# Kernel optimization log

Measured on AMD Instinct MI355X. Metric: run time of the kernel, lower is better.

## Reference

```python
import jax, jax.numpy as jnp
import numpy as np

B, S, I, H = 1024, 200, 4, 128  # batch, seq_len, interest_num, hidden_size
ROUTING_TIMES = 3
EPS = 1e-9


def setup_inputs() -> dict:
    key = jax.random.key(0)
    k1, k2, k3 = jax.random.split(key, 3)
    item_eb = jax.random.normal(k1, (B, S, H), dtype=jnp.float32)
    mask = jax.random.randint(k2, (B, S), 0, 2, dtype=jnp.int32)
    w = jax.random.normal(k3, (1, S, I * H, H), dtype=jnp.float32)
    return {"item_eb": item_eb, "mask": mask, "w": w}


def _squash_factor(cap):
    # cap: [B, I, 1, H]; standard capsule squash scale
    n = jnp.sum(jnp.square(cap), axis=-1, keepdims=True)
    return n / (1.0 + n) / jnp.sqrt(n + EPS)


def reference(item_eb, mask, w):
    # bilinear_type == 2: item_eb_hat[b,s,i] = sum_h w[0,s,i,h] * item_eb[b,s,h]
    hat = jnp.einsum('bsh,sjh->bsj', item_eb, w[0])          # [B, S, I*H]
    hat = hat.reshape(B, S, I, H).transpose(0, 2, 1, 3)      # [B, I, S, H]
    hat_iter = jax.lax.stop_gradient(hat)                    # stop_grad=True

    atten_mask = mask[:, None, :]                            # [B, 1, S] broadcasts over I
    capsule_weight = jnp.zeros((B, I, S), dtype=item_eb.dtype)

    interest_capsule = None
    for i in range(ROUTING_TIMES):
        sw = jax.nn.softmax(capsule_weight, axis=-1)         # [B, I, S]
        sw = jnp.where(atten_mask == 0, jnp.zeros_like(sw), sw)
        sw = sw[:, :, None, :]                               # [B, I, 1, S]
        src = hat_iter if i < ROUTING_TIMES - 1 else hat
        interest_capsule = jnp.matmul(sw, src)               # [B, I, 1, H]
        interest_capsule = _squash_factor(interest_capsule) * interest_capsule
        if i < ROUTING_TIMES - 1:
            # delta[b,i,s] = <hat_iter[b,i,s,:], capsule[b,i,0,:]>
            delta = jnp.matmul(hat_iter, jnp.swapaxes(interest_capsule, 2, 3))
            capsule_weight = capsule_weight + delta.reshape(B, I, S)

    return interest_capsule.reshape(B, I, H)
```

## Files before the change

### kernel.cpp

```cpp
#include <hip/hip_runtime.h>
#include <hip/hip_bf16.h>
#include <cstdint>

#define SDIM 200
#define HDIM 128
#define IDIM 4
#define BDIM 1024
#define LDK 72
#define REG_US 9216
#define HALF_US 18432
#define IMG_US 36864

typedef __attribute__((ext_vector_type(8))) short short8;
typedef __attribute__((ext_vector_type(4))) float f32x4;

__device__ __forceinline__ ushort f32_to_bf16u(float f) {
    uint32_t u = __builtin_bit_cast(uint32_t, f);
    u += 0x7FFFu + ((u >> 16) & 1u);
    return (ushort)(u >> 16);
}
__device__ __forceinline__ float bf16u_to_f32(ushort h) {
    uint32_t u = ((uint32_t)h) << 16;
    return __builtin_bit_cast(float, u);
}
__device__ __forceinline__ void split8(const float* p, uint4* hi, uint4* lo) {
    union { ushort u[8]; uint4 v; } xh, xl;
    #pragma unroll
    for (int j = 0; j < 8; ++j) {
        float f = p[j];
        ushort h = f32_to_bf16u(f);
        float r = f - bf16u_to_f32(h);
        xh.u[j] = h;
        xl.u[j] = f32_to_bf16u(r);
    }
    *hi = xh.v; *lo = xl.v;
}

__global__ __launch_bounds__(256) void wstage(const float* __restrict__ w,
                                              ushort* __restrict__ img) {
    const int blk = blockIdx.x;
    const int s = blk >> 2, ii = blk & 3;
    const int t = threadIdx.x;
    const float* wB = w + ((size_t)s * (IDIM * HDIM) + (size_t)ii * HDIM) * HDIM;
    ushort* dst = img + (size_t)blk * IMG_US;

    for (int g = t; g < 2048; g += 256) {
        uint4 hi, lo;
        split8(wB + (size_t)g * 8, &hi, &lo);
        int c0 = g >> 4;
        int st = (g >> 3) & 1;
        int kl = (g & 7) * 8;
        *(uint4*)(dst + st * HALF_US +          c0 * LDK + kl) = hi;
        *(uint4*)(dst + st * HALF_US + REG_US + c0 * LDK + kl) = lo;
    }
    for (int p = t; p < 4096; p += 256) {
        int rg = p >> 10, c0 = (p >> 3) & 127, o = p & 7;
        dst[rg * REG_US + c0 * LDK + 64 + o] = 0;
    }
}

__global__ __launch_bounds__(256) void hat_gemm(const float* __restrict__ item,
                                                const ushort* __restrict__ img,
                                                float* __restrict__ hat,
                                                int b0) {
    __shared__ ushort lds[HALF_US];

    const int blk = blockIdx.x;
    const int bt = blk / SDIM;
    const int s  = blk % SDIM;
    const int t  = threadIdx.x;
    const int wave = t >> 6, lane = t & 63;
    const int wm = wave >> 1, wn = wave & 1;
    const int m0 = lane & 15, q = lane >> 4;

    short8 ah[2][2][4], al[2][2][4];
    const float* ib = item +
        ((size_t)(b0 + bt * 128 + wm * 64 + m0) * SDIM + s) * HDIM;
    #pragma unroll
    for (int tm = 0; tm < 4; ++tm) {
        const float* p = ib + (size_t)(tm * 16) * (SDIM * HDIM);
        #pragma unroll
        for (int st = 0; st < 2; ++st)
            #pragma unroll
            for (int kk = 0; kk < 2; ++kk) {
                uint4 hi, lo;
                split8(p + st * 64 + kk * 32 + q * 8, &hi, &lo);
                ah[st][kk][tm] = __builtin_bit_cast(short8, hi);
                al[st][kk][tm] = __builtin_bit_cast(short8, lo);
            }
    }

    const ushort* imgS = img + (size_t)(s * IDIM) * IMG_US;

    #pragma unroll 1
    for (int ii = 0; ii < IDIM; ++ii) {
        const ushort* wimg = imgS + (size_t)ii * IMG_US;

        f32x4 acc[4][4];
        #pragma unroll
        for (int tm = 0; tm < 4; ++tm)
            #pragma unroll
            for (int tn = 0; tn < 4; ++tn)
                acc[tm][tn] = (f32x4){0.f, 0.f, 0.f, 0.f};

        #pragma unroll
        for (int st = 0; st < 2; ++st) {
            __syncthreads();

            {
                const uint4* src = (const uint4*)(wimg + (size_t)st * HALF_US);
                uint4* dstl = (uint4*)lds;
                #pragma unroll
                for (int k = 0; k < 9; ++k)
                    dstl[t + 256 * k] = src[t + 256 * k];
            }
            __syncthreads();

            const ushort* Wh = lds;
            const ushort* Wl = lds + REG_US;
            #pragma unroll
            for (int kk = 0; kk < 2; ++kk) {
                const int kof = kk * 32 + q * 8;
                short8 bh[4], bl[4];
                #pragma unroll
                for (int tn = 0; tn < 4; ++tn) {
                    int ro = (wn * 64 + tn * 16 + m0) * LDK + kof;
                    bh[tn] = *(const short8*)(&Wh[ro]);
                    bl[tn] = *(const short8*)(&Wl[ro]);
                }
                #pragma unroll
                for (int tm = 0; tm < 4; ++tm)
                    #pragma unroll
                    for (int tn = 0; tn < 4; ++tn) {
                        acc[tm][tn] = __builtin_amdgcn_mfma_f32_16x16x32_bf16(
                            ah[st][kk][tm], bl[tn], acc[tm][tn], 0, 0, 0);
                        acc[tm][tn] = __builtin_amdgcn_mfma_f32_16x16x32_bf16(
                            al[st][kk][tm], bh[tn], acc[tm][tn], 0, 0, 0);
                        acc[tm][tn] = __builtin_amdgcn_mfma_f32_16x16x32_bf16(
                            ah[st][kk][tm], bh[tn], acc[tm][tn], 0, 0, 0);
                    }
            }
        }

        #pragma unroll
        for (int tm = 0; tm < 4; ++tm) {
            #pragma unroll
            for (int tn = 0; tn < 4; ++tn) {
                const int col = wn * 64 + tn * 16 + m0;
                #pragma unroll
                for (int rg = 0; rg < 4; ++rg) {
                    const size_t bl_ = (size_t)(bt * 128 + wm * 64 + tm * 16 + q * 4 + rg);
                    hat[((bl_ * IDIM + ii) * SDIM + s) * HDIM + col] = acc[tm][tn][rg];
                }
            }
        }
    }
}

__global__ __launch_bounds__(512) void routing4(const float* __restrict__ hat,
                                                const int* __restrict__ mask,
                                                float* __restrict__ out, int b0) {
    __shared__ float cw[SDIM];
    __shared__ float icp[16 * HDIM];
    __shared__ float icf[HDIM];
    __shared__ int   mk[SDIM];

    const int blk = blockIdx.x;
    const int bl = blk >> 2, ii = blk & 3;
    const int b = b0 + bl;
    const int t = threadIdx.x, lane = t & 63, wv = t >> 6;
    const int hq = (t & 31) * 4;
    const int sg = t >> 5;
    const bool has13 = (sg < 8);
    const float* base = hat + ((size_t)bl * IDIM + ii) * (SDIM * HDIM);

    if (t < SDIM) mk[t] = mask[(size_t)b * SDIM + t];

    float4 pf[13];
    #pragma unroll
    for (int j = 0; j < 12; ++j)
        pf[j] = *(const float4*)(base + (size_t)(sg + 16 * j) * HDIM + hq);
    pf[12] = has13 ? *(const float4*)(base + (size_t)(sg + 192) * HDIM + hq)
                   : (float4){0.f, 0.f, 0.f, 0.f};
    __syncthreads();

    {
        float4 u = {0.f, 0.f, 0.f, 0.f};
        #pragma unroll
        for (int j = 0; j < 12; ++j) {
            if (mk[sg + 16 * j]) {
                u.x += pf[j].x; u.y += pf[j].y; u.z += pf[j].z; u.w += pf[j].w;
            }
        }
        if (has13 && mk[sg + 192]) {
            u.x += pf[12].x; u.y += pf[12].y; u.z += pf[12].z; u.w += pf[12].w;
        }
        *(float4*)(&icp[sg * HDIM + hq]) = u;
    }
    __syncthreads();
    {
        float i0 = 0.f, i1 = 0.f;
        #pragma unroll
        for (int g = 0; g < 16; ++g) {
            i0 += icp[g * HDIM + lane];
            i1 += icp[g * HDIM + lane + 64];
        }
        i0 *= (1.0f / 200.0f);
        i1 *= (1.0f / 200.0f);
        float p = i0 * i0 + i1 * i1;
        #pragma unroll
        for (int off = 32; off > 0; off >>= 1) p += __shfl_xor(p, off);
        float fac = p / (1.0f + p) / sqrtf(p + 1e-9f);
        if (wv == 0) {
            icf[lane] = i0 * fac;
            icf[lane + 64] = i1 * fac;
        }
    }
    __syncthreads();

    for (int iter = 1; iter <= 2; ++iter) {
        float4 c4 = *(const float4*)(&icf[hq]);
        #pragma unroll
        for (int j = 0; j < 13; ++j) {
            float d = fmaf(pf[j].x, c4.x, fmaf(pf[j].y, c4.y,
                      fmaf(pf[j].z, c4.z, pf[j].w * c4.w)));
            d += __shfl_xor(d, 16);
            d += __shfl_xor(d, 8);
            d += __shfl_xor(d, 4);
            d += __shfl_xor(d, 2);
            d += __shfl_xor(d, 1);
            if ((t & 31) == 0 && (j < 12 || has13)) {
                int s = sg + 16 * j;
                cw[s] = (iter == 1) ? d : cw[s] + d;
            }
        }
        __syncthreads();

        float m = fmaxf(cw[lane], fmaxf(cw[lane + 64], cw[lane + 128]));
        if (lane < SDIM - 192) m = fmaxf(m, cw[lane + 192]);
        #pragma unroll
        for (int off = 32; off > 0; off >>= 1) m = fmaxf(m, __shfl_xor(m, off));

        float D = __expf(cw[lane] - m) + __expf(cw[lane + 64] - m)
                + __expf(cw[lane + 128] - m)
                + ((lane < SDIM - 192) ? __expf(cw[lane + 192] - m) : 0.0f);
        #pragma unroll
        for (int off = 32; off > 0; off >>= 1) D += __shfl_xor(D, off);

        {
            float4 u = {0.f, 0.f, 0.f, 0.f};
            #pragma unroll
            for (int j = 0; j < 12; ++j) {
                int s = sg + 16 * j;
                float wgt = mk[s] ? __expf(cw[s] - m) : 0.0f;
                u.x = fmaf(wgt, pf[j].x, u.x);
                u.y = fmaf(wgt, pf[j].y, u.y);
                u.z = fmaf(wgt, pf[j].z, u.z);
                u.w = fmaf(wgt, pf[j].w, u.w);
            }
            float wgt = (has13 && mk[sg + 192]) ? __expf(cw[sg + 192] - m) : 0.0f;
            u.x = fmaf(wgt, pf[12].x, u.x);
            u.y = fmaf(wgt, pf[12].y, u.y);
            u.z = fmaf(wgt, pf[12].z, u.z);
            u.w = fmaf(wgt, pf[12].w, u.w);
            *(float4*)(&icp[sg * HDIM + hq]) = u;
        }
        __syncthreads();

        {
            float i0 = 0.f, i1 = 0.f;
            #pragma unroll
            for (int g = 0; g < 16; ++g) {
                i0 += icp[g * HDIM + lane];
                i1 += icp[g * HDIM + lane + 64];
            }
            i0 /= D;
            i1 /= D;
            float p = i0 * i0 + i1 * i1;
            #pragma unroll
            for (int off = 32; off > 0; off >>= 1) p += __shfl_xor(p, off);
            float fac = p / (1.0f + p) / sqrtf(p + 1e-9f);
            if (iter == 1) {
                if (wv == 0) {
                    icf[lane] = i0 * fac;
                    icf[lane + 64] = i1 * fac;
                }
            } else {
                if (wv == 0) {
                    out[((size_t)b * IDIM + ii) * HDIM + lane]      = i0 * fac;
                    out[((size_t)b * IDIM + ii) * HDIM + lane + 64] = i1 * fac;
                }
            }
        }
        if (iter == 1) __syncthreads();
    }
}

extern "C" void kernel_launch(void* const* d_in, const int* in_sizes, int n_in,
                              void* d_out, int out_size, void* d_ws, size_t ws_size,
                              hipStream_t stream) {
    const float* item = nullptr;
    const int*   msk  = nullptr;
    const float* w    = nullptr;
    for (int i = 0; i < n_in; ++i) {
        if (in_sizes[i] == BDIM * SDIM * HDIM)             item = (const float*)d_in[i];
        else if (in_sizes[i] == BDIM * SDIM)               msk  = (const int*)d_in[i];
        else if (in_sizes[i] == SDIM * IDIM * HDIM * HDIM) w    = (const float*)d_in[i];
    }
    if (!item) item = (const float*)d_in[0];
    if (!msk)  msk  = (const int*)d_in[1];
    if (!w)    w    = (const float*)d_in[2];

    const size_t imgBytes = (size_t)SDIM * IDIM * IMG_US * sizeof(ushort);
    ushort* wimg = (ushort*)d_ws;
    float*  hat  = (float*)((char*)d_ws + imgBytes);
    float*  out  = (float*)d_out;

    wstage<<<SDIM * IDIM, 256, 0, stream>>>(w, wimg);

    const size_t perB = (size_t)IDIM * SDIM * HDIM * sizeof(float);
    size_t hatCap = (ws_size - imgBytes) / perB;
    int chunk = 512;
    if (hatCap < (size_t)chunk) chunk = (int)((hatCap / 128) * 128);
    if (chunk < 128) chunk = 128;
    for (int bb = 0; bb < BDIM; bb += chunk) {
        int cb = (BDIM - bb < chunk) ? (BDIM - bb) : chunk;
        int nbt = cb / 128;
        hat_gemm<<<nbt * SDIM, 256, 0, stream>>>(item, wimg, hat, bb);
        routing4<<<cb * IDIM, 512, 0, stream>>>(hat, msk, out, bb);
    }
}
```

Before: 510.6 us.

## Double-buffer weight image in LDS using direct global-to-LDS async loads

```diff
diff --git a/kernel.cpp b/kernel.cpp
--- a/kernel.cpp
+++ b/kernel.cpp
@@ -36,6 +36,13 @@
     *hi = xh.v; *lo = xl.v;
 }
 
+__device__ __forceinline__ void gload16(const void* g, void* l) {
+    __builtin_amdgcn_global_load_lds(
+        (const __attribute__((address_space(1))) void*)g,
+        (__attribute__((address_space(3))) void*)l,
+        16, 0, 0);
+}
+
 __global__ __launch_bounds__(256) void wstage(const float* __restrict__ w,
                                               ushort* __restrict__ img) {
     const int blk = blockIdx.x;
@@ -53,9 +60,10 @@
         *(uint4*)(dst + st * HALF_US +          c0 * LDK + kl) = hi;
         *(uint4*)(dst + st * HALF_US + REG_US + c0 * LDK + kl) = lo;
     }
-    for (int p = t; p < 4096; p += 256) {
-        int rg = p >> 10, c0 = (p >> 3) & 127, o = p & 7;
-        dst[rg * REG_US + c0 * LDK + 64 + o] = 0;
+    const uint4 z = {0u, 0u, 0u, 0u};
+    for (int p = t; p < 512; p += 256) {
+        int rg = p >> 7, c0 = p & 127;
+        *(uint4*)(dst + rg * REG_US + c0 * LDK + 64) = z;
     }
 }
 
@@ -63,7 +71,7 @@
                                                 const ushort* __restrict__ img,
                                                 float* __restrict__ hat,
                                                 int b0) {
-    __shared__ ushort lds[HALF_US];
+    __shared__ ushort lds[2 * HALF_US];
 
     const int blk = blockIdx.x;
     const int bt = blk / SDIM;
@@ -73,88 +81,103 @@
     const int wm = wave >> 1, wn = wave & 1;
     const int m0 = lane & 15, q = lane >> 4;
 
+    const ushort* imgS = img + (size_t)(s * IDIM) * IMG_US;
+
+    #define STAGE(dstbuf, srcp)                                            \
+        {                                                                  \
+            const char* _s = (const char*)(srcp);                          \
+            char* _d = (char*)(dstbuf);                                    \
+            _Pragma("unroll")                                              \
+            for (int _i = 0; _i < 9; ++_i) {                               \
+                const int _off = (_i * 256 + wave * 64) * 16;              \
+                gload16(_s + _off + lane * 16, _d + _off);                 \
+            }                                                              \
+        }
+
+    STAGE(lds, imgS);
+
     short8 ah[2][2][4], al[2][2][4];
-    const float* ib = item +
-        ((size_t)(b0 + bt * 128 + wm * 64 + m0) * SDIM + s) * HDIM;
+    {
+        const float* ib = item +
+            ((size_t)(b0 + bt * 128 + wm * 64 + m0) * SDIM + s) * HDIM;
+        #pragma unroll
+        for (int tm = 0; tm < 4; ++tm) {
+            const float* p = ib + (size_t)(tm * 16) * (SDIM * HDIM);
+            #pragma unroll
+            for (int st = 0; st < 2; ++st)
+                #pragma unroll
+                for (int kk = 0; kk < 2; ++kk) {
+                    uint4 hi, lo;
+                    split8(p + st * 64 + kk * 32 + q * 8, &hi, &lo);
+                    ah[st][kk][tm] = __builtin_bit_cast(short8, hi);
+                    al[st][kk][tm] = __builtin_bit_cast(short8, lo);
+                }
+        }
+    }
+    __syncthreads();
+
+    f32x4 acc[4][4];
+
     #pragma unroll
-    for (int tm = 0; tm < 4; ++tm) {
-        const float* p = ib + (size_t)(tm * 16) * (SDIM * HDIM);
-        #pragma unroll
-        for (int st = 0; st < 2; ++st)
-            #pragma unroll
-            for (int kk = 0; kk < 2; ++kk) {
-                uint4 hi, lo;
-                split8(p + st * 64 + kk * 32 + q * 8, &hi, &lo);
-                ah[st][kk][tm] = __builtin_bit_cast(short8, hi);
-                al[st][kk][tm] = __builtin_bit_cast(short8, lo);
-            }
-    }
-
-    const ushort* imgS = img + (size_t)(s * IDIM) * IMG_US;
-
-    #pragma unroll 1
-    for (int ii = 0; ii < IDIM; ++ii) {
-        const ushort* wimg = imgS + (size_t)ii * IMG_US;
-
-        f32x4 acc[4][4];
-        #pragma unroll
-        for (int tm = 0; tm < 4; ++tm)
-            #pragma unroll
-            for (int tn = 0; tn < 4; ++tn)
-                acc[tm][tn] = (f32x4){0.f, 0.f, 0.f, 0.f};
-
-        #pragma unroll
-        for (int st = 0; st < 2; ++st) {
-            __syncthreads();
-
-            {
-                const uint4* src = (const uint4*)(wimg + (size_t)st * HALF_US);
-                uint4* dstl = (uint4*)lds;
+    for (int k = 0; k < 8; ++k) {
+        const int ii = k >> 1, st = k & 1;
+
+        if (st == 0) {
+            #pragma unroll
+            for (int tm = 0; tm < 4; ++tm)
                 #pragma unroll
-                for (int k = 0; k < 9; ++k)
-                    dstl[t + 256 * k] = src[t + 256 * k];
-            }
-            __syncthreads();
-
-            const ushort* Wh = lds;
-            const ushort* Wl = lds + REG_US;
-            #pragma unroll
-            for (int kk = 0; kk < 2; ++kk) {
-                const int kof = kk * 32 + q * 8;
-                short8 bh[4], bl[4];
+                for (int tn = 0; tn < 4; ++tn)
+                    acc[tm][tn] = (f32x4){0.f, 0.f, 0.f, 0.f};
+        }
+
+        if (k < 7)
+            STAGE(lds + ((k + 1) & 1) * HALF_US, imgS + (size_t)(k + 1) * HALF_US);
+
+        const ushort* Wh = lds + (k & 1) * HALF_US;
+        const ushort* Wl = Wh + REG_US;
+        #pragma unroll
+        for (int kk = 0; kk < 2; ++kk) {
+            const int kof = kk * 32 + q * 8;
+            short8 bh[4], bl[4];
+            #pragma unroll
+            for (int tn = 0; tn < 4; ++tn) {
+                int ro = (wn * 64 + tn * 16 + m0) * LDK + kof;
+                bh[tn] = *(const short8*)(&Wh[ro]);
+                bl[tn] = *(const short8*)(&Wl[ro]);
+            }
+            #pragma unroll
+            for (int tm = 0; tm < 4; ++tm)
                 #pragma unroll
                 for (int tn = 0; tn < 4; ++tn) {
-                    int ro = (wn * 64 + tn * 16 + m0) * LDK + kof;
-                    bh[tn] = *(const short8*)(&Wh[ro]);
-                    bl[tn] = *(const short8*)(&Wl[ro]);
-                }
+                    acc[tm][tn] = __builtin_amdgcn_mfma_f32_16x16x32_bf16(
+                        ah[st][kk][tm], bl[tn], acc[tm][tn], 0, 0, 0);
+                    acc[tm][tn] = __builtin_amdgcn_mfma_f32_16x16x32_bf16(
+                        al[st][kk][tm], bh[tn], acc[tm][tn], 0, 0, 0);
+                    acc[tm][tn] = __builtin_amdgcn_mfma_f32_16x16x32_bf16(
+                        ah[st][kk][tm], bh[tn], acc[tm][tn], 0, 0, 0);
+                }
+        }
+
+        if (st == 1) {
+            #pragma unroll
+            for (int tm = 0; tm < 4; ++tm) {
                 #pragma unroll
-                for (int tm = 0; tm < 4; ++tm)
+                for (int tn = 0; tn < 4; ++tn) {
+                    const int col = wn * 64 + tn * 16 + m0;
                     #pragma unroll
-                    for (int tn = 0; tn < 4; ++tn) {
-                        acc[tm][tn] = __builtin_amdgcn_mfma_f32_16x16x32_bf16(
-                            ah[st][kk][tm], bl[tn], acc[tm][tn], 0, 0, 0);
-                        acc[tm][tn] = __builtin_amdgcn_mfma_f32_16x16x32_bf16(
-                            al[st][kk][tm], bh[tn], acc[tm][tn], 0, 0, 0);
-                        acc[tm][tn] = __builtin_amdgcn_mfma_f32_16x16x32_bf16(
-                            ah[st][kk][tm], bh[tn], acc[tm][tn], 0, 0, 0);
+                    for (int rg = 0; rg < 4; ++rg) {
+                        const size_t bl_ =
+                            (size_t)(bt * 128 + wm * 64 + tm * 16 + q * 4 + rg);
+                        hat[((bl_ * IDIM + ii) * SDIM + s) * HDIM + col] =
+                            acc[tm][tn][rg];
                     }
-            }
-        }
-
-        #pragma unroll
-        for (int tm = 0; tm < 4; ++tm) {
-            #pragma unroll
-            for (int tn = 0; tn < 4; ++tn) {
-                const int col = wn * 64 + tn * 16 + m0;
-                #pragma unroll
-                for (int rg = 0; rg < 4; ++rg) {
-                    const size_t bl_ = (size_t)(bt * 128 + wm * 64 + tm * 16 + q * 4 + rg);
-                    hat[((bl_ * IDIM + ii) * SDIM + s) * HDIM + col] = acc[tm][tn][rg];
-                }
-            }
-        }
-    }
+                }
+            }
+        }
+
+        if (k < 7) __syncthreads();
+    }
+    #undef STAGE
 }
 
 __global__ __launch_bounds__(512) void routing4(const float* __restrict__ hat,
```

After: 495.9 us. -2.9%, faster.

## Shrink hat_gemm batch tile to 32 rows and stage weights via direct global-to-LDS loads

Applied to the files above, without the earlier changes.

```diff
diff --git a/kernel.cpp b/kernel.cpp
--- a/kernel.cpp
+++ b/kernel.cpp
@@ -36,6 +36,13 @@
     *hi = xh.v; *lo = xl.v;
 }
 
+__device__ __forceinline__ void gload16(const void* g, void* l) {
+    __builtin_amdgcn_global_load_lds(
+        (const __attribute__((address_space(1))) void*)g,
+        (__attribute__((address_space(3))) void*)l,
+        16, 0, 0);
+}
+
 __global__ __launch_bounds__(256) void wstage(const float* __restrict__ w,
                                               ushort* __restrict__ img) {
     const int blk = blockIdx.x;
@@ -53,54 +60,54 @@
         *(uint4*)(dst + st * HALF_US +          c0 * LDK + kl) = hi;
         *(uint4*)(dst + st * HALF_US + REG_US + c0 * LDK + kl) = lo;
     }
-    for (int p = t; p < 4096; p += 256) {
-        int rg = p >> 10, c0 = (p >> 3) & 127, o = p & 7;
-        dst[rg * REG_US + c0 * LDK + 64 + o] = 0;
-    }
-}
-
-__global__ __launch_bounds__(256) void hat_gemm(const float* __restrict__ item,
-                                                const ushort* __restrict__ img,
-                                                float* __restrict__ hat,
-                                                int b0) {
+    const uint4 z = {0u, 0u, 0u, 0u};
+    for (int p = t; p < 512; p += 256) {
+        int rg = p >> 7, c0 = p & 127;
+        *(uint4*)(dst + rg * REG_US + c0 * LDK + 64) = z;
+    }
+}
+
+__global__ __launch_bounds__(256, 4) void hat_gemm(const float* __restrict__ item,
+                                                   const ushort* __restrict__ img,
+                                                   float* __restrict__ hat,
+                                                   int b0, int nbt) {
     __shared__ ushort lds[HALF_US];
 
     const int blk = blockIdx.x;
-    const int bt = blk / SDIM;
-    const int s  = blk % SDIM;
+    const int s  = blk / nbt;
+    const int bt = blk % nbt;
     const int t  = threadIdx.x;
-    const int wave = t >> 6, lane = t & 63;
-    const int wm = wave >> 1, wn = wave & 1;
+    const int wn = t >> 6, lane = t & 63;
     const int m0 = lane & 15, q = lane >> 4;
 
-    short8 ah[2][2][4], al[2][2][4];
-    const float* ib = item +
-        ((size_t)(b0 + bt * 128 + wm * 64 + m0) * SDIM + s) * HDIM;
-    #pragma unroll
-    for (int tm = 0; tm < 4; ++tm) {
-        const float* p = ib + (size_t)(tm * 16) * (SDIM * HDIM);
-        #pragma unroll
-        for (int st = 0; st < 2; ++st)
-            #pragma unroll
-            for (int kk = 0; kk < 2; ++kk) {
-                uint4 hi, lo;
-                split8(p + st * 64 + kk * 32 + q * 8, &hi, &lo);
-                ah[st][kk][tm] = __builtin_bit_cast(short8, hi);
-                al[st][kk][tm] = __builtin_bit_cast(short8, lo);
-            }
+    short8 ah[2][2][2], al[2][2][2];
+    {
+        const float* ib = item +
+            ((size_t)(b0 + bt * 32 + m0) * SDIM + s) * HDIM;
+        #pragma unroll
+        for (int tm = 0; tm < 2; ++tm) {
+            const float* p = ib + (size_t)(tm * 16) * (SDIM * HDIM);
+            #pragma unroll
+            for (int st = 0; st < 2; ++st)
+                #pragma unroll
+                for (int kk = 0; kk < 2; ++kk) {
+                    uint4 hi, lo;
+                    split8(p + st * 64 + kk * 32 + q * 8, &hi, &lo);
+                    ah[st][kk][tm] = __builtin_bit_cast(short8, hi);
+                    al[st][kk][tm] = __builtin_bit_cast(short8, lo);
+                }
+        }
     }
 
     const ushort* imgS = img + (size_t)(s * IDIM) * IMG_US;
 
     #pragma unroll 1
     for (int ii = 0; ii < IDIM; ++ii) {
-        const ushort* wimg = imgS + (size_t)ii * IMG_US;
-
-        f32x4 acc[4][4];
-        #pragma unroll
-        for (int tm = 0; tm < 4; ++tm)
-            #pragma unroll
-            for (int tn = 0; tn < 4; ++tn)
+        f32x4 acc[2][2];
+        #pragma unroll
+        for (int tm = 0; tm < 2; ++tm)
+            #pragma unroll
+            for (int tn = 0; tn < 2; ++tn)
                 acc[tm][tn] = (f32x4){0.f, 0.f, 0.f, 0.f};
 
         #pragma unroll
@@ -108,11 +115,14 @@
             __syncthreads();
 
             {
-                const uint4* src = (const uint4*)(wimg + (size_t)st * HALF_US);
-                uint4* dstl = (uint4*)lds;
-                #pragma unroll
-                for (int k = 0; k < 9; ++k)
-                    dstl[t + 256 * k] = src[t + 256 * k];
+                const char* src = (const char*)(imgS + (size_t)ii * IMG_US
+                                                + (size_t)st * HALF_US);
+                char* dst = (char*)lds;
+                #pragma unroll
+                for (int i = 0; i < 9; ++i) {
+                    const int off = (i * 256 + wn * 64) * 16;
+                    gload16(src + off + lane * 16, dst + off);
+                }
             }
             __syncthreads();
 
@@ -121,19 +131,19 @@
             #pragma unroll
             for (int kk = 0; kk < 2; ++kk) {
                 const int kof = kk * 32 + q * 8;
-                short8 bh[4], bl[4];
-                #pragma unroll
-                for (int tn = 0; tn < 4; ++tn) {
-                    int ro = (wn * 64 + tn * 16 + m0) * LDK + kof;
-                    bh[tn] = *(const short8*)(&Wh[ro]);
-                    bl[tn] = *(const short8*)(&Wl[ro]);
-                }
-                #pragma unroll
-                for (int tm = 0; tm < 4; ++tm)
+                short8 bh[2], bl2[2];
+                #pragma unroll
+                for (int tn = 0; tn < 2; ++tn) {
+                    int ro = (wn * 32 + tn * 16 + m0) * LDK + kof;
+                    bh[tn]  = *(const short8*)(&Wh[ro]);
+                    bl2[tn] = *(const short8*)(&Wl[ro]);
+                }
+                #pragma unroll
+                for (int tm = 0; tm < 2; ++tm)
                     #pragma unroll
-                    for (int tn = 0; tn < 4; ++tn) {
+                    for (int tn = 0; tn < 2; ++tn) {
                         acc[tm][tn] = __builtin_amdgcn_mfma_f32_16x16x32_bf16(
-                            ah[st][kk][tm], bl[tn], acc[tm][tn], 0, 0, 0);
+                            ah[st][kk][tm], bl2[tn], acc[tm][tn], 0, 0, 0);
                         acc[tm][tn] = __builtin_amdgcn_mfma_f32_16x16x32_bf16(
                             al[st][kk][tm], bh[tn], acc[tm][tn], 0, 0, 0);
                         acc[tm][tn] = __builtin_amdgcn_mfma_f32_16x16x32_bf16(
@@ -143,14 +153,15 @@
         }
 
         #pragma unroll
-        for (int tm = 0; tm < 4; ++tm) {
-            #pragma unroll
-            for (int tn = 0; tn < 4; ++tn) {
-                const int col = wn * 64 + tn * 16 + m0;
+        for (int tm = 0; tm < 2; ++tm) {
+            #pragma unroll
+            for (int tn = 0; tn < 2; ++tn) {
+                const int col = wn * 32 + tn * 16 + m0;
                 #pragma unroll
                 for (int rg = 0; rg < 4; ++rg) {
-                    const size_t bl_ = (size_t)(bt * 128 + wm * 64 + tm * 16 + q * 4 + rg);
-                    hat[((bl_ * IDIM + ii) * SDIM + s) * HDIM + col] = acc[tm][tn][rg];
+                    const size_t bl_ = (size_t)(bt * 32 + tm * 16 + q * 4 + rg);
+                    hat[((bl_ * IDIM + ii) * SDIM + s) * HDIM + col] =
+                        acc[tm][tn][rg];
                 }
             }
         }
@@ -325,8 +336,8 @@
     if (chunk < 128) chunk = 128;
     for (int bb = 0; bb < BDIM; bb += chunk) {
         int cb = (BDIM - bb < chunk) ? (BDIM - bb) : chunk;
-        int nbt = cb / 128;
-        hat_gemm<<<nbt * SDIM, 256, 0, stream>>>(item, wimg, hat, bb);
+        int nbt = cb / 32;
+        hat_gemm<<<SDIM * nbt, 256, 0, stream>>>(item, wimg, hat, bb, nbt);
         routing4<<<cb * IDIM, 512, 0, stream>>>(hat, msk, out, bb);
     }
 }
```

Result: slower. 625.3 us (+22.5%).
